# Performance work log

Measured on AMD Instinct MI355X. Metric: run time of the kernel, lower is better.

Reference implementation:

```python
import jax, jax.numpy as jnp
import numpy as np

EMB = 384
HEADS = 6
QDIM = 64
DFF = 4 * EMB
EPS = 1e-5


def layer_norm(x, g, b):
    mu = jnp.mean(x, axis=-1, keepdims=True)
    var = jnp.mean((x - mu) ** 2, axis=-1, keepdims=True)
    return (x - mu) * jax.lax.rsqrt(var + EPS) * g + b


def setup_inputs() -> dict:
    key = jax.random.key(0)
    ks = jax.random.split(key, 12)
    s = EMB ** -0.5
    return {
        "x": jax.random.normal(ks[0], (32, 512, EMB), dtype=jnp.float32),
        "Wq": jax.random.normal(ks[1], (EMB, EMB), dtype=jnp.float32) * s,
        "Wk": jax.random.normal(ks[2], (EMB, EMB), dtype=jnp.float32) * s,
        "Wv": jax.random.normal(ks[3], (EMB, EMB), dtype=jnp.float32) * s,
        "Wp": jax.random.normal(ks[4], (EMB, EMB), dtype=jnp.float32) * s,
        "bp": jnp.zeros((EMB,), dtype=jnp.float32),
        "g1": jnp.ones((EMB,), dtype=jnp.float32),
        "b1": jnp.zeros((EMB,), dtype=jnp.float32),
        "g2": jnp.ones((EMB,), dtype=jnp.float32),
        "b2": jnp.zeros((EMB,), dtype=jnp.float32),
        "W1": jax.random.normal(ks[5], (EMB, DFF), dtype=jnp.float32) * s,
        "bf1": jnp.zeros((DFF,), dtype=jnp.float32),
        "W2": jax.random.normal(ks[6], (DFF, EMB), dtype=jnp.float32) * (DFF ** -0.5),
        "bf2": jnp.zeros((EMB,), dtype=jnp.float32),
    }


def reference(x, Wq, Wk, Wv, Wp, bp, g1, b1, g2, b2, W1, bf1, W2, bf2):
    B, T, C = x.shape
    # --- self-attention on ln1(x) ---
    h = layer_norm(x, g1, b1)
    q = (h @ Wq).reshape(B, T, HEADS, QDIM).transpose(0, 2, 1, 3)  # [B,H,T,D]
    k = (h @ Wk).reshape(B, T, HEADS, QDIM).transpose(0, 2, 1, 3)
    v = (h @ Wv).reshape(B, T, HEADS, QDIM).transpose(0, 2, 1, 3)
    aff = jnp.einsum('bhtd,bhsd->bhts', q, k) * (QDIM ** -0.5)  # [B,H,T,T]
    causal = jnp.tril(jnp.ones((T, T), dtype=bool))
    aff = jnp.where(causal, aff, -jnp.inf)
    aff = jax.nn.softmax(aff, axis=-1)
    o = jnp.einsum('bhts,bhsd->bhtd', aff, v)
    o = o.transpose(0, 2, 1, 3).reshape(B, T, C)
    x = x + (o @ Wp + bp)
    # --- feed-forward on ln2(x) ---
    h2 = layer_norm(x, g2, b2)
    ff = jax.nn.relu(h2 @ W1 + bf1) @ W2 + bf2
    return x + ff
```

## Files before the change

kernel.cpp:

```cpp
#include <hip/hip_runtime.h>
#include <cstdint>
#include <cstddef>

#define DEVINL __device__ __forceinline__

typedef short short8 __attribute__((ext_vector_type(8)));
typedef float f32x4 __attribute__((ext_vector_type(4)));
typedef unsigned short ushort;
typedef ushort u16x8 __attribute__((ext_vector_type(8)));
typedef ushort u16x4 __attribute__((ext_vector_type(4)));

DEVINL float bf2f(ushort u) {
  union { unsigned int i; float f; } v; v.i = ((unsigned int)u) << 16; return v.f;
}
DEVINL ushort f2bf(float f) {
  union { float f; unsigned int i; } v; v.f = f;
  unsigned int u = v.i;
  unsigned int r = u + 0x7fffu + ((u >> 16) & 1u);
  return (ushort)(r >> 16);
}

DEVINL void gl2lds16(const ushort* g, ushort* l) {
  __builtin_amdgcn_global_load_lds(
      (const __attribute__((address_space(1))) void*)g,
      (__attribute__((address_space(3))) void*)l, 16, 0, 0);
}

__global__ void transpose4_k(const float* __restrict__ i0, const float* __restrict__ i1,
                             const float* __restrict__ i2, const float* __restrict__ i3,
                             ushort* __restrict__ o0, ushort* __restrict__ o1,
                             ushort* __restrict__ o2, ushort* __restrict__ o3) {
  __shared__ float tile[32][33];
  int z = blockIdx.z;
  const float* in = (z == 0) ? i0 : (z == 1) ? i1 : (z == 2) ? i2 : i3;
  ushort* out = (z == 0) ? o0 : (z == 1) ? o1 : (z == 2) ? o2 : o3;
  int bx = blockIdx.x, by = blockIdx.y;
  int tx = threadIdx.x, ty = threadIdx.y;
  int x = bx * 32 + tx;
#pragma unroll
  for (int i = 0; i < 4; i++) {
    int y = by * 32 + ty + i * 8;
    tile[ty + i * 8][tx] = in[(size_t)y * 384 + x];
  }
  __syncthreads();
  int x2 = by * 32 + tx;
#pragma unroll
  for (int i = 0; i < 4; i++) {
    int y2 = bx * 32 + ty + i * 8;
    out[(size_t)y2 * 384 + x2] = f2bf(tile[tx][ty + i * 8]);
  }
}

__global__ void transpose_k(const float* __restrict__ in, ushort* __restrict__ out,
                            int R, int C) {
  __shared__ float tile[32][33];
  int bx = blockIdx.x, by = blockIdx.y;
  int tx = threadIdx.x, ty = threadIdx.y;
  int x = bx * 32 + tx;
#pragma unroll
  for (int i = 0; i < 4; i++) {
    int y = by * 32 + ty + i * 8;
    tile[ty + i * 8][tx] = in[(size_t)y * C + x];
  }
  __syncthreads();
  int x2 = by * 32 + tx;
#pragma unroll
  for (int i = 0; i < 4; i++) {
    int y2 = bx * 32 + ty + i * 8;
    out[(size_t)y2 * R + x2] = f2bf(tile[tx][ty + i * 8]);
  }
}

__global__ __launch_bounds__(256) void ln_k(const float* __restrict__ x,
                                            const float* __restrict__ g,
                                            const float* __restrict__ b,
                                            ushort* __restrict__ out) {
  int wave = threadIdx.x >> 6;
  int lane = threadIdx.x & 63;
  int row = blockIdx.x * 4 + wave;
  const float* xr = x + (size_t)row * 384;
  float v[6];
#pragma unroll
  for (int j = 0; j < 3; j++) {
    float2 p = *(const float2*)(xr + lane * 2 + j * 128);
    v[2 * j] = p.x;
    v[2 * j + 1] = p.y;
  }
  float s = v[0] + v[1] + v[2] + v[3] + v[4] + v[5];
#pragma unroll
  for (int off = 32; off; off >>= 1) s += __shfl_xor(s, off);
  float mu = s * (1.0f / 384.0f);
  float s2 = 0.f;
#pragma unroll
  for (int j = 0; j < 6; j++) { float d = v[j] - mu; s2 += d * d; }
#pragma unroll
  for (int off = 32; off; off >>= 1) s2 += __shfl_xor(s2, off);
  float rs = rsqrtf(s2 * (1.0f / 384.0f) + 1e-5f);
  ushort* orow = out + (size_t)row * 384;
#pragma unroll
  for (int j = 0; j < 3; j++) {
    int c = lane * 2 + j * 128;
    float2 pg = *(const float2*)(g + c);
    float2 pb = *(const float2*)(b + c);
    float y0 = (v[2 * j] - mu) * rs * pg.x + pb.x;
    float y1 = (v[2 * j + 1] - mu) * rs * pg.y + pb.y;
    uint32_t po = (uint32_t)f2bf(y0) | ((uint32_t)f2bf(y1) << 16);
    *(uint32_t*)(orow + c) = po;
  }
}

template <int MODE, int TN>
__global__ __launch_bounds__(256) void gemm_k(
    const ushort* __restrict__ A, int K,
    const ushort* __restrict__ WTa, const ushort* __restrict__ WTb,
    const ushort* __restrict__ WTc,
    const float* __restrict__ bias, const float* residf,
    ushort* __restrict__ outa, ushort* __restrict__ outb,
    ushort* __restrict__ outc, float* outf) {
  constexpr int NJ = TN / 32;
  __shared__ __align__(16) ushort As[128 * 64];
  __shared__ __align__(16) ushort Bs[TN * 64];
  int tid = threadIdx.x;
  int lane = tid & 63, wave = tid >> 6;
  int wm = wave & 1, wn = wave >> 1;
  int q4 = lane >> 4, ln16 = lane & 15;
  int rowBase = blockIdx.x * 128;
  int colBase = blockIdx.y * TN;

  const ushort* WT;
  if (MODE == 0) {
    int z = blockIdx.z;
    WT = (z == 0) ? WTa : (z == 1) ? WTb : WTc;
  } else {
    WT = WTa;
  }

  f32x4 acc[4][NJ];
#pragma unroll
  for (int i = 0; i < 4; i++)
#pragma unroll
    for (int j = 0; j < NJ; j++) acc[i][j] = (f32x4){0.f, 0.f, 0.f, 0.f};

  int ri = lane >> 3;
  int g8 = (lane & 7) ^ ri;

  for (int kb = 0; kb < K; kb += 64) {
#pragma unroll
    for (int h = 0; h < 128; h += 32) {
      int base = h + wave * 8;
      gl2lds16(&A[(size_t)(rowBase + base + ri) * K + kb + g8 * 8], &As[base * 64]);
    }
#pragma unroll
    for (int h = 0; h < TN; h += 32) {
      int base = h + wave * 8;
      gl2lds16(&WT[(size_t)(colBase + base + ri) * K + kb + g8 * 8], &Bs[base * 64]);
    }
    __syncthreads();
#pragma unroll
    for (int ks = 0; ks < 2; ks++) {
      short8 af[4], bfr[NJ];
#pragma unroll
      for (int i = 0; i < 4; i++) {
        int ar = wm * 64 + i * 16 + ln16;
        int slot = (ks * 4 + q4) ^ (ar & 7);
        af[i] = *(const short8*)&As[ar * 64 + slot * 8];
      }
#pragma unroll
      for (int j = 0; j < NJ; j++) {
        int br = wn * (TN / 2) + j * 16 + ln16;
        int slot = (ks * 4 + q4) ^ (br & 7);
        bfr[j] = *(const short8*)&Bs[br * 64 + slot * 8];
      }
#pragma unroll
      for (int i = 0; i < 4; i++)
#pragma unroll
        for (int j = 0; j < NJ; j++)
          acc[i][j] = __builtin_amdgcn_mfma_f32_16x16x32_bf16(af[i], bfr[j], acc[i][j], 0, 0, 0);
    }
    __syncthreads();
  }

#pragma unroll
  for (int i = 0; i < 4; i++) {
#pragma unroll
    for (int j = 0; j < NJ; j++) {
      int row0 = rowBase + wm * 64 + i * 16 + q4 * 4;
      int col = colBase + wn * (TN / 2) + j * 16 + ln16;
      if (MODE == 0) {
        int z = blockIdx.z;
        if (z < 2) {
          ushort* o = (z == 0) ? outa : outb;
#pragma unroll
          for (int r = 0; r < 4; r++) {
            int row = row0 + r;
            int bb = row >> 9, t = row & 511, h = col >> 6, d = col & 63;
            o[(((size_t)(bb * 6 + h) * 512) + t) * 64 + d] = f2bf(acc[i][j][r]);
          }
        } else {
          int bb = row0 >> 9, t0 = row0 & 511, h = col >> 6, d = col & 63;
          u16x4 pk = {f2bf(acc[i][j][0]), f2bf(acc[i][j][1]), f2bf(acc[i][j][2]),
                      f2bf(acc[i][j][3])};
          *(u16x4*)&outc[(((size_t)(bb * 6 + h) * 64) + d) * 512 + t0] = pk;
        }
      } else if (MODE == 1) {
        float bcol = bias[col];
#pragma unroll
        for (int r = 0; r < 4; r++) {
          size_t idx = (size_t)(row0 + r) * 384 + col;
          outf[idx] = acc[i][j][r] + bcol + residf[idx];
        }
      } else {
        float bcol = bias[col];
#pragma unroll
        for (int r = 0; r < 4; r++) {
          size_t idx = (size_t)(row0 + r) * 1536 + col;
          float vv = acc[i][j][r] + bcol;
          outa[idx] = f2bf(vv > 0.f ? vv : 0.f);
        }
      }
    }
  }
}

__global__ __launch_bounds__(256) void attn_k(const ushort* __restrict__ qg,
                                              const ushort* __restrict__ kg,
                                              const ushort* __restrict__ vtg,
                                              ushort* __restrict__ outg) {
  __shared__ ushort Ks[64][88];
  __shared__ ushort VTs[64][88];
  __shared__ ushort Pw[4][16][88];
  int tid = threadIdx.x, lane = tid & 63, wave = tid >> 6;
  int l = blockIdx.x;
  int xcd = l & 7, m = l >> 3;
  int bh = xcd * 24 + (m >> 2);
  int pr = m & 3;
  int lo = pr, hi = 7 - pr;
  int quad = lane >> 4, ln16 = lane & 15;

  const ushort* qp = qg + (size_t)bh * 512 * 64;
  const ushort* kp = kg + (size_t)bh * 512 * 64;
  const ushort* vp = vtg + (size_t)bh * 64 * 512;

  int t_lo = lo * 64 + wave * 16 + ln16;
  int t_hi = hi * 64 + wave * 16 + ln16;
  short8 bqlo0 = *(const short8*)&qp[(size_t)t_lo * 64 + quad * 8];
  short8 bqlo1 = *(const short8*)&qp[(size_t)t_lo * 64 + 32 + quad * 8];
  short8 bqhi0 = *(const short8*)&qp[(size_t)t_hi * 64 + quad * 8];
  short8 bqhi1 = *(const short8*)&qp[(size_t)t_hi * 64 + 32 + quad * 8];

  f32x4 Olo[4], Ohi[4];
#pragma unroll
  for (int dt = 0; dt < 4; dt++) {
    Olo[dt] = (f32x4){0.f, 0.f, 0.f, 0.f};
    Ohi[dt] = (f32x4){0.f, 0.f, 0.f, 0.f};
  }
  float m_lo = -3.0e38f, l_lo = 0.f, m_hi = -3.0e38f, l_hi = 0.f;

  const float SC = 0.125f * 1.44269504088896f;

  auto process = [&](short8 q0f, short8 q1f, int t_row, float& m_, float& l_,
                     f32x4* O, int s0) {
    f32x4 St[4];
#pragma unroll
    for (int kt = 0; kt < 4; kt++) {
      short8 a0 = *(const short8*)&Ks[kt * 16 + ln16][quad * 8];
      short8 a1 = *(const short8*)&Ks[kt * 16 + ln16][32 + quad * 8];
      f32x4 z = (f32x4){0.f, 0.f, 0.f, 0.f};
      z = __builtin_amdgcn_mfma_f32_16x16x32_bf16(a0, q0f, z, 0, 0, 0);
      z = __builtin_amdgcn_mfma_f32_16x16x32_bf16(a1, q1f, z, 0, 0, 0);
      St[kt] = z;
    }
#pragma unroll
    for (int kt = 0; kt < 4; kt++)
#pragma unroll
      for (int r = 0; r < 4; r++) {
        int s_abs = s0 + kt * 16 + quad * 4 + r;
        float vv = St[kt][r] * SC;
        St[kt][r] = (s_abs <= t_row) ? vv : -3.0e38f;
      }
    float vm = St[0][0];
#pragma unroll
    for (int kt = 0; kt < 4; kt++)
#pragma unroll
      for (int r = 0; r < 4; r++) vm = fmaxf(vm, St[kt][r]);
    vm = fmaxf(vm, __shfl_xor(vm, 16));
    vm = fmaxf(vm, __shfl_xor(vm, 32));
    float mn = fmaxf(m_, vm);
    float alpha = exp2f(m_ - mn);
    m_ = mn;
    float ps = 0.f;
#pragma unroll
    for (int kt = 0; kt < 4; kt++)
#pragma unroll
      for (int r = 0; r < 4; r++) {
        float p = exp2f(St[kt][r] - mn);
        St[kt][r] = p;
        ps += p;
      }
    ps += __shfl_xor(ps, 16);
    ps += __shfl_xor(ps, 32);
    l_ = l_ * alpha + ps;
#pragma unroll
    for (int dt = 0; dt < 4; dt++)
#pragma unroll
      for (int r = 0; r < 4; r++) O[dt][r] *= alpha;

    asm volatile("" ::: "memory");
#pragma unroll
    for (int kt = 0; kt < 4; kt++) {
      u16x4 pk = {f2bf(St[kt][0]), f2bf(St[kt][1]), f2bf(St[kt][2]), f2bf(St[kt][3])};
      *(u16x4*)&Pw[wave][ln16][kt * 16 + quad * 4] = pk;
    }
    asm volatile("" ::: "memory");
    union { u16x8 u; short8 s; } p0, p1;
    p0.u = *(const u16x8*)&Pw[wave][ln16][quad * 8];
    p1.u = *(const u16x8*)&Pw[wave][ln16][32 + quad * 8];
#pragma unroll
    for (int dt = 0; dt < 4; dt++) {
      short8 v0 = *(const short8*)&VTs[dt * 16 + ln16][quad * 8];
      short8 v1 = *(const short8*)&VTs[dt * 16 + ln16][32 + quad * 8];
      O[dt] = __builtin_amdgcn_mfma_f32_16x16x32_bf16(v0, p0.s, O[dt], 0, 0, 0);
      O[dt] = __builtin_amdgcn_mfma_f32_16x16x32_bf16(v1, p1.s, O[dt], 0, 0, 0);
    }
  };

  for (int s0 = 0; s0 <= hi * 64; s0 += 64) {
    {
      int r = tid >> 2;
      int c0 = (tid & 3) * 8;
#pragma unroll
      for (int p = 0; p < 2; p++) {
        int c = c0 + p * 32;
        *(u16x8*)&Ks[r][c] = *(const u16x8*)&kp[(size_t)(s0 + r) * 64 + c];
        *(u16x8*)&VTs[r][c] = *(const u16x8*)&vp[(size_t)r * 512 + s0 + c];
      }
    }
    __syncthreads();
    if (s0 <= lo * 64) process(bqlo0, bqlo1, t_lo, m_lo, l_lo, Olo, s0);
    process(bqhi0, bqhi1, t_hi, m_hi, l_hi, Ohi, s0);
    __syncthreads();
  }

  int b = bh / 6, h = bh % 6;
  float ilo = 1.0f / l_lo, ihi = 1.0f / l_hi;
  size_t base_lo = ((size_t)(b * 512) + t_lo) * 384 + h * 64;
  size_t base_hi = ((size_t)(b * 512) + t_hi) * 384 + h * 64;
#pragma unroll
  for (int dt = 0; dt < 4; dt++) {
    u16x4 plo = {f2bf(Olo[dt][0] * ilo), f2bf(Olo[dt][1] * ilo),
                 f2bf(Olo[dt][2] * ilo), f2bf(Olo[dt][3] * ilo)};
    *(u16x4*)&outg[base_lo + dt * 16 + quad * 4] = plo;
    u16x4 phi = {f2bf(Ohi[dt][0] * ihi), f2bf(Ohi[dt][1] * ihi),
                 f2bf(Ohi[dt][2] * ihi), f2bf(Ohi[dt][3] * ihi)};
    *(u16x4*)&outg[base_hi + dt * 16 + quad * 4] = phi;
  }
}

extern "C" void kernel_launch(void* const* d_in, const int* in_sizes, int n_in,
                              void* d_out, int out_size, void* d_ws, size_t ws_size,
                              hipStream_t stream) {
  const float* x = (const float*)d_in[0];
  const float* Wq = (const float*)d_in[1];
  const float* Wk = (const float*)d_in[2];
  const float* Wv = (const float*)d_in[3];
  const float* Wp = (const float*)d_in[4];
  const float* bp = (const float*)d_in[5];
  const float* g1 = (const float*)d_in[6];
  const float* b1 = (const float*)d_in[7];
  const float* g2 = (const float*)d_in[8];
  const float* b2 = (const float*)d_in[9];
  const float* W1 = (const float*)d_in[10];
  const float* bf1 = (const float*)d_in[11];
  const float* W2 = (const float*)d_in[12];
  const float* bf2 = (const float*)d_in[13];
  float* outp = (float*)d_out;

  char* ws = (char*)d_ws;
  size_t off = 0;
  auto alloc = [&](size_t elems) {
    ushort* p = (ushort*)(ws + off);
    off += elems * 2;
    return p;
  };
  ushort* WqT = alloc((size_t)384 * 384);
  ushort* WkT = alloc((size_t)384 * 384);
  ushort* WvT = alloc((size_t)384 * 384);
  ushort* WpT = alloc((size_t)384 * 384);
  ushort* W1T = alloc((size_t)384 * 1536);
  ushort* W2T = alloc((size_t)1536 * 384);
  ushort* bufq = alloc((size_t)16384 * 384);
  ushort* m1 = alloc((size_t)16384 * 1536);
  ushort* h1_attn = m1;
  ushort* bufk = m1 + (size_t)16384 * 384;
  ushort* vT = m1 + (size_t)2 * 16384 * 384;

  dim3 tb(32, 8);
  transpose4_k<<<dim3(12, 12, 4), tb, 0, stream>>>(Wq, Wk, Wv, Wp, WqT, WkT, WvT, WpT);
  transpose_k<<<dim3(48, 12), tb, 0, stream>>>(W1, W1T, 384, 1536);
  transpose_k<<<dim3(12, 48), tb, 0, stream>>>(W2, W2T, 1536, 384);

  ln_k<<<4096, 256, 0, stream>>>(x, g1, b1, h1_attn);
  gemm_k<0, 128><<<dim3(128, 3, 3), 256, 0, stream>>>(
      h1_attn, 384, WqT, WkT, WvT, nullptr, nullptr, bufq, bufk, vT, nullptr);
  attn_k<<<768, 256, 0, stream>>>(bufq, bufk, vT, h1_attn);
  gemm_k<1, 64><<<dim3(128, 6), 256, 0, stream>>>(
      h1_attn, 384, WpT, nullptr, nullptr, bp, x, nullptr, nullptr, nullptr, outp);
  ln_k<<<4096, 256, 0, stream>>>(outp, g2, b2, bufq);
  gemm_k<2, 128><<<dim3(128, 12), 256, 0, stream>>>(
      bufq, 384, W1T, nullptr, nullptr, bf1, nullptr, m1, nullptr, nullptr, nullptr);
  gemm_k<1, 64><<<dim3(128, 6), 256, 0, stream>>>(
      m1, 1536, W2T, nullptr, nullptr, bf2, outp, nullptr, nullptr, nullptr, outp);
}
```

Baseline: 265.0 us.

## Rework attention tile loads, masking, rescaling and fuse weight transposes

```diff
diff --git a/kernel.cpp b/kernel.cpp
--- a/kernel.cpp
+++ b/kernel.cpp
@@ -26,35 +26,27 @@
       (__attribute__((address_space(3))) void*)l, 16, 0, 0);
 }
 
-__global__ void transpose4_k(const float* __restrict__ i0, const float* __restrict__ i1,
-                             const float* __restrict__ i2, const float* __restrict__ i3,
-                             ushort* __restrict__ o0, ushort* __restrict__ o1,
-                             ushort* __restrict__ o2, ushort* __restrict__ o3) {
+__global__ void transpose6_k(const float* __restrict__ Wq, const float* __restrict__ Wk,
+                             const float* __restrict__ Wv, const float* __restrict__ Wp,
+                             const float* __restrict__ W1, const float* __restrict__ W2,
+                             ushort* __restrict__ WqT, ushort* __restrict__ WkT,
+                             ushort* __restrict__ WvT, ushort* __restrict__ WpT,
+                             ushort* __restrict__ W1T, ushort* __restrict__ W2T) {
   __shared__ float tile[32][33];
   int z = blockIdx.z;
-  const float* in = (z == 0) ? i0 : (z == 1) ? i1 : (z == 2) ? i2 : i3;
-  ushort* out = (z == 0) ? o0 : (z == 1) ? o1 : (z == 2) ? o2 : o3;
-  int bx = blockIdx.x, by = blockIdx.y;
-  int tx = threadIdx.x, ty = threadIdx.y;
-  int x = bx * 32 + tx;
-#pragma unroll
-  for (int i = 0; i < 4; i++) {
-    int y = by * 32 + ty + i * 8;
-    tile[ty + i * 8][tx] = in[(size_t)y * 384 + x];
-  }
-  __syncthreads();
-  int x2 = by * 32 + tx;
-#pragma unroll
-  for (int i = 0; i < 4; i++) {
-    int y2 = bx * 32 + ty + i * 8;
-    out[(size_t)y2 * 384 + x2] = f2bf(tile[tx][ty + i * 8]);
-  }
-}
-
-__global__ void transpose_k(const float* __restrict__ in, ushort* __restrict__ out,
-                            int R, int C) {
-  __shared__ float tile[32][33];
-  int bx = blockIdx.x, by = blockIdx.y;
+  const float* in;
+  ushort* out;
+  int R, C, bx, by;
+  if (z < 4) {
+    if (blockIdx.x >= 12) return;
+    in = (z == 0) ? Wq : (z == 1) ? Wk : (z == 2) ? Wv : Wp;
+    out = (z == 0) ? WqT : (z == 1) ? WkT : (z == 2) ? WvT : WpT;
+    R = 384; C = 384; bx = blockIdx.x; by = blockIdx.y;
+  } else if (z == 4) {
+    in = W1; out = W1T; R = 384; C = 1536; bx = blockIdx.x; by = blockIdx.y;
+  } else {
+    in = W2; out = W2T; R = 1536; C = 384; bx = blockIdx.y; by = blockIdx.x;
+  }
   int tx = threadIdx.x, ty = threadIdx.y;
   int x = bx * 32 + tx;
 #pragma unroll
@@ -189,12 +181,13 @@
       if (MODE == 0) {
         int z = blockIdx.z;
         if (z < 2) {
+          float sc = (z == 0) ? 0.18033688011112f : 1.0f;
           ushort* o = (z == 0) ? outa : outb;
 #pragma unroll
           for (int r = 0; r < 4; r++) {
             int row = row0 + r;
             int bb = row >> 9, t = row & 511, h = col >> 6, d = col & 63;
-            o[(((size_t)(bb * 6 + h) * 512) + t) * 64 + d] = f2bf(acc[i][j][r]);
+            o[(((size_t)(bb * 6 + h) * 512) + t) * 64 + d] = f2bf(acc[i][j][r] * sc);
           }
         } else {
           int bb = row0 >> 9, t0 = row0 & 511, h = col >> 6, d = col & 63;
@@ -226,9 +219,9 @@
                                               const ushort* __restrict__ kg,
                                               const ushort* __restrict__ vtg,
                                               ushort* __restrict__ outg) {
-  __shared__ ushort Ks[64][88];
-  __shared__ ushort VTs[64][88];
-  __shared__ ushort Pw[4][16][88];
+  __shared__ __align__(16) ushort Ks[64 * 64];
+  __shared__ __align__(16) ushort VTs[64 * 64];
+  __shared__ __align__(16) ushort Pw[4][16][88];
   int tid = threadIdx.x, lane = tid & 63, wave = tid >> 6;
   int l = blockIdx.x;
   int xcd = l & 7, m = l >> 3;
@@ -236,10 +229,16 @@
   int pr = m & 3;
   int lo = pr, hi = 7 - pr;
   int quad = lane >> 4, ln16 = lane & 15;
+  int x7 = ln16 & 7;
+  int slo = (quad ^ x7) * 8;
+  int shi = slo ^ 32;
 
   const ushort* qp = qg + (size_t)bh * 512 * 64;
   const ushort* kp = kg + (size_t)bh * 512 * 64;
   const ushort* vp = vtg + (size_t)bh * 64 * 512;
+
+  int ri = lane >> 3;
+  int g8 = (lane & 7) ^ ri;
 
   int t_lo = lo * 64 + wave * 16 + ln16;
   int t_hi = hi * 64 + wave * 16 + ln16;
@@ -256,28 +255,30 @@
   }
   float m_lo = -3.0e38f, l_lo = 0.f, m_hi = -3.0e38f, l_hi = 0.f;
 
-  const float SC = 0.125f * 1.44269504088896f;
-
   auto process = [&](short8 q0f, short8 q1f, int t_row, float& m_, float& l_,
-                     f32x4* O, int s0) {
+                     f32x4* O, int s0, bool maskit) {
     f32x4 St[4];
+    __builtin_amdgcn_s_setprio(1);
 #pragma unroll
     for (int kt = 0; kt < 4; kt++) {
-      short8 a0 = *(const short8*)&Ks[kt * 16 + ln16][quad * 8];
-      short8 a1 = *(const short8*)&Ks[kt * 16 + ln16][32 + quad * 8];
+      int r = kt * 16 + ln16;
+      short8 a0 = *(const short8*)&Ks[r * 64 + slo];
+      short8 a1 = *(const short8*)&Ks[r * 64 + shi];
       f32x4 z = (f32x4){0.f, 0.f, 0.f, 0.f};
       z = __builtin_amdgcn_mfma_f32_16x16x32_bf16(a0, q0f, z, 0, 0, 0);
       z = __builtin_amdgcn_mfma_f32_16x16x32_bf16(a1, q1f, z, 0, 0, 0);
       St[kt] = z;
     }
-#pragma unroll
-    for (int kt = 0; kt < 4; kt++)
-#pragma unroll
-      for (int r = 0; r < 4; r++) {
-        int s_abs = s0 + kt * 16 + quad * 4 + r;
-        float vv = St[kt][r] * SC;
-        St[kt][r] = (s_abs <= t_row) ? vv : -3.0e38f;
-      }
+    __builtin_amdgcn_s_setprio(0);
+    if (maskit) {
+#pragma unroll
+      for (int kt = 0; kt < 4; kt++)
+#pragma unroll
+        for (int r = 0; r < 4; r++) {
+          int s_abs = s0 + kt * 16 + quad * 4 + r;
+          St[kt][r] = (s_abs <= t_row) ? St[kt][r] : -3.0e38f;
+        }
+    }
     float vm = St[0][0];
 #pragma unroll
     for (int kt = 0; kt < 4; kt++)
@@ -286,24 +287,27 @@
     vm = fmaxf(vm, __shfl_xor(vm, 16));
     vm = fmaxf(vm, __shfl_xor(vm, 32));
     float mn = fmaxf(m_, vm);
-    float alpha = exp2f(m_ - mn);
-    m_ = mn;
+    if (!__all(mn - m_ <= 8.0f)) {
+      float alpha = exp2f(m_ - mn);
+      m_ = mn;
+      l_ *= alpha;
+#pragma unroll
+      for (int dt = 0; dt < 4; dt++)
+#pragma unroll
+        for (int r = 0; r < 4; r++) O[dt][r] *= alpha;
+    }
     float ps = 0.f;
 #pragma unroll
     for (int kt = 0; kt < 4; kt++)
 #pragma unroll
       for (int r = 0; r < 4; r++) {
-        float p = exp2f(St[kt][r] - mn);
+        float p = exp2f(St[kt][r] - m_);
         St[kt][r] = p;
         ps += p;
       }
     ps += __shfl_xor(ps, 16);
     ps += __shfl_xor(ps, 32);
-    l_ = l_ * alpha + ps;
-#pragma unroll
-    for (int dt = 0; dt < 4; dt++)
-#pragma unroll
-      for (int r = 0; r < 4; r++) O[dt][r] *= alpha;
+    l_ += ps;
 
     asm volatile("" ::: "memory");
 #pragma unroll
@@ -315,29 +319,28 @@
     union { u16x8 u; short8 s; } p0, p1;
     p0.u = *(const u16x8*)&Pw[wave][ln16][quad * 8];
     p1.u = *(const u16x8*)&Pw[wave][ln16][32 + quad * 8];
+    __builtin_amdgcn_s_setprio(1);
 #pragma unroll
     for (int dt = 0; dt < 4; dt++) {
-      short8 v0 = *(const short8*)&VTs[dt * 16 + ln16][quad * 8];
-      short8 v1 = *(const short8*)&VTs[dt * 16 + ln16][32 + quad * 8];
+      int r = dt * 16 + ln16;
+      short8 v0 = *(const short8*)&VTs[r * 64 + slo];
+      short8 v1 = *(const short8*)&VTs[r * 64 + shi];
       O[dt] = __builtin_amdgcn_mfma_f32_16x16x32_bf16(v0, p0.s, O[dt], 0, 0, 0);
       O[dt] = __builtin_amdgcn_mfma_f32_16x16x32_bf16(v1, p1.s, O[dt], 0, 0, 0);
     }
+    __builtin_amdgcn_s_setprio(0);
   };
 
   for (int s0 = 0; s0 <= hi * 64; s0 += 64) {
-    {
-      int r = tid >> 2;
-      int c0 = (tid & 3) * 8;
-#pragma unroll
-      for (int p = 0; p < 2; p++) {
-        int c = c0 + p * 32;
-        *(u16x8*)&Ks[r][c] = *(const u16x8*)&kp[(size_t)(s0 + r) * 64 + c];
-        *(u16x8*)&VTs[r][c] = *(const u16x8*)&vp[(size_t)r * 512 + s0 + c];
-      }
+#pragma unroll
+    for (int h = 0; h < 64; h += 32) {
+      int base = h + wave * 8;
+      gl2lds16(&kp[(size_t)(s0 + base + ri) * 64 + g8 * 8], &Ks[base * 64]);
+      gl2lds16(&vp[(size_t)(base + ri) * 512 + s0 + g8 * 8], &VTs[base * 64]);
     }
     __syncthreads();
-    if (s0 <= lo * 64) process(bqlo0, bqlo1, t_lo, m_lo, l_lo, Olo, s0);
-    process(bqhi0, bqhi1, t_hi, m_hi, l_hi, Ohi, s0);
+    if (s0 <= lo * 64) process(bqlo0, bqlo1, t_lo, m_lo, l_lo, Olo, s0, s0 == lo * 64);
+    process(bqhi0, bqhi1, t_hi, m_hi, l_hi, Ohi, s0, s0 == hi * 64);
     __syncthreads();
   }
 
@@ -395,9 +398,8 @@
   ushort* vT = m1 + (size_t)2 * 16384 * 384;
 
   dim3 tb(32, 8);
-  transpose4_k<<<dim3(12, 12, 4), tb, 0, stream>>>(Wq, Wk, Wv, Wp, WqT, WkT, WvT, WpT);
-  transpose_k<<<dim3(48, 12), tb, 0, stream>>>(W1, W1T, 384, 1536);
-  transpose_k<<<dim3(12, 48), tb, 0, stream>>>(W2, W2T, 1536, 384);
+  transpose6_k<<<dim3(48, 12, 6), tb, 0, stream>>>(Wq, Wk, Wv, Wp, W1, W2,
+                                                   WqT, WkT, WvT, WpT, W1T, W2T);
 
   ln_k<<<4096, 256, 0, stream>>>(x, g1, b1, h1_attn);
   gemm_k<0, 128><<<dim3(128, 3, 3), 256, 0, stream>>>(
```

After: 248.0 us. -6.4%, faster.
